# Performance work log

Hardware: AMD Instinct MI355X
Metric: run time of the kernel (lower is better)

Reference implementation:

```python
import jax, jax.numpy as jnp
import numpy as np
import math

B, T, D, NH, HD = 2, 1024, 768, 12, 64
V, L, E, CAP_F, H = 50257, 2, 8, 1.25, 2048
AUX_W, Z_W, THETA, EPS = 0.01, 0.001, 10000.0, 1e-5
N = B * T
CAP = int(math.ceil(N / E * CAP_F))  # 320


def setup_inputs():
    key = jax.random.key(0)
    ks = jax.random.split(key, 8)
    s = 0.02
    return dict(
        idx=jax.random.randint(ks[0], (B, T), 0, V),
        wte=jax.random.normal(ks[1], (V, D), jnp.float32) * s,
        wqkv=jax.random.normal(ks[2], (L, D, 3 * D), jnp.float32) * s,
        q_norm_w=jnp.ones((L, D), jnp.float32),
        k_norm_w=jnp.ones((L, D), jnp.float32),
        o_proj=jax.random.normal(ks[3], (L, D, D), jnp.float32) * s,
        ffn_norm_w=jnp.ones((L, D), jnp.float32),
        gate_w=jax.random.normal(ks[4], (L, D, E), jnp.float32) * s,
        w13=jax.random.normal(ks[5], (L, E, D, 2 * H), jnp.float32) * s,
        w2=jax.random.normal(ks[6], (L, E, H, D), jnp.float32) * s,
        ln_f_w=jnp.ones((D,), jnp.float32),
    )


def rmsnorm(x, w):
    return x * jax.lax.rsqrt(jnp.mean(x * x, axis=-1, keepdims=True) + EPS) * w


def rope(x, cos, sin):
    # x: (B, nh, T, HD) viewed as complex pairs on last dim
    xr = x.reshape(*x.shape[:-1], HD // 2, 2)
    x0, x1 = xr[..., 0], xr[..., 1]
    out = jnp.stack([x0 * cos - x1 * sin, x0 * sin + x1 * cos], axis=-1)
    return out.reshape(x.shape)


def moe(x, gate_w, w13, w2):
    # x: (B, T, D) -> Switch MoE (k=1) with capacity CAP and token drops
    x_flat = x.reshape(N, D).astype(jnp.float32)
    logits = x_flat @ gate_w  # (N, E) fp32
    probs = jax.nn.softmax(logits, axis=-1)
    top = jnp.argmax(logits, axis=-1)  # (N,)
    prob_mass = probs.mean(axis=0)
    fraction = jax.nn.one_hot(top, E, dtype=jnp.float32).mean(axis=0)
    balance_loss = jnp.sum(prob_mass * fraction) * AUX_W * E
    z = jax.nn.logsumexp(logits, axis=-1)
    z_loss = jnp.mean(z * z) * Z_W
    aux = balance_loss + z_loss

    sort_idx = jnp.argsort(top)  # stable
    sorted_assign = top[sort_idx]
    counts = jnp.bincount(sorted_assign, length=E)
    offsets = jnp.concatenate([jnp.zeros((1,), counts.dtype), jnp.cumsum(counts)])[:E]
    rank = jnp.arange(N) - offsets[sorted_assign]  # position within expert segment
    keep = rank < CAP
    x_perm = x_flat[sort_idx]
    slot = jnp.where(keep, rank, CAP)  # dropped -> overflow slot
    buf = jnp.zeros((E, CAP + 1, D), jnp.float32).at[sorted_assign, slot].set(x_perm)
    xb = buf[:, :CAP]  # (E, CAP, D)
    gu = jnp.einsum('ecd,edh->ech', xb, w13)  # (E, CAP, 2H)
    g, u = jnp.split(gu, 2, axis=-1)
    y = jnp.einsum('ech,ehd->ecd', jax.nn.silu(g) * u, w2)  # (E, CAP, D)
    out_perm = y[sorted_assign, jnp.minimum(rank, CAP - 1)] * keep[:, None]
    out_flat = jnp.zeros((N, D), jnp.float32).at[sort_idx].set(out_perm)
    return out_flat.reshape(B, T, D), aux, top.reshape(B, T), keep[jnp.argsort(sort_idx)].reshape(B, T)


def forward(idx, wte, wqkv, q_norm_w, k_norm_w, o_proj, ffn_norm_w, gate_w, w13, w2, ln_f_w):
    x = wte[idx]  # (B, T, D)
    freqs = 1.0 / (THETA ** (jnp.arange(0, HD, 2, dtype=jnp.float32) / HD))
    ang = jnp.outer(jnp.arange(T, dtype=jnp.float32), freqs)  # (T, HD//2)
    cos, sin = jnp.cos(ang)[None, None], jnp.sin(ang)[None, None]
    mask = jnp.where(jnp.tril(jnp.ones((T, T), bool)), 0.0, -jnp.inf)
    aux_total = jnp.float32(0.0)
    for l in range(L):
        qkv = x @ wqkv[l]
        q, k, v = jnp.split(qkv, 3, axis=-1)
        q = rmsnorm(q, q_norm_w[l])
        k = rmsnorm(k, k_norm_w[l])
        q = q.reshape(B, T, NH, HD).transpose(0, 2, 1, 3)
        k = k.reshape(B, T, NH, HD).transpose(0, 2, 1, 3)
        v = v.reshape(B, T, NH, HD).transpose(0, 2, 1, 3)
        q, k = rope(q, cos, sin), rope(k, cos, sin)
        scores = jnp.einsum('bhqd,bhkd->bhqk', q, k) / math.sqrt(HD) + mask
        attn = jax.nn.softmax(scores, axis=-1)
        y = jnp.einsum('bhqk,bhkd->bhqd', attn, v).transpose(0, 2, 1, 3).reshape(B, T, D)
        h = x + y @ o_proj[l]
        ffn_in = rmsnorm(h, ffn_norm_w[l])
        moe_out, aux, _, _ = moe(ffn_in, gate_w[l], w13[l], w2[l])
        aux_total = aux_total + aux
        x = h + moe_out
    x = rmsnorm(x, ln_f_w)
    logits = x @ wte.T  # tied lm_head
    return logits, aux_total


def reference(idx, wte, wqkv, q_norm_w, k_norm_w, o_proj, ffn_norm_w, gate_w, w13, w2, ln_f_w):
    return forward(idx, wte, wqkv, q_norm_w, k_norm_w, o_proj, ffn_norm_w, gate_w, w13, w2, ln_f_w)
```

## Files before the change

kernel.cpp:

```cpp
#include <hip/hip_runtime.h>

typedef __attribute__((ext_vector_type(8))) _Float16 half8;
typedef __attribute__((ext_vector_type(4))) float f32x4;

constexpr int Bc = 2, Tc = 1024, Dc = 768, NHc = 12, HDc = 64;
constexpr int Vc = 50257, Lc = 2, Ec = 8, Hc = 2048;
constexpr int Ntok = Bc * Tc;
constexpr int CAPc = 320, CAPPc = 384;
constexpr long long LOGITS_N = (long long)Bc * Tc * Vc;

typedef const __attribute__((address_space(1))) unsigned int* gas_t;
typedef __attribute__((address_space(3))) unsigned int* las_t;
__device__ __forceinline__ void gload16(const void* g, void* l) {
  __builtin_amdgcn_global_load_lds((gas_t)g, (las_t)l, 16, 0, 0);
}

__device__ __forceinline__ void splitf16(float a, unsigned short& h, unsigned short& l) {
  _Float16 hh = (_Float16)a;
  _Float16 ll = (_Float16)(a - (float)hh);
  h = __builtin_bit_cast(unsigned short, hh);
  l = __builtin_bit_cast(unsigned short, ll);
}
__device__ __forceinline__ unsigned short f16o(float a) {
  _Float16 hh = (_Float16)a;
  return __builtin_bit_cast(unsigned short, hh);
}


__global__ void zero_small(float* psum, float* z2) {
  int t = threadIdx.x;
  if (t < Lc * Ec) psum[t] = 0.f;
  if (t < Lc) z2[t] = 0.f;
}

__global__ void embed_k(const int* __restrict__ idx, const float* __restrict__ wte,
                        float* __restrict__ x, unsigned short* __restrict__ x16) {
  int n = blockIdx.x;
  long long v = idx[n];
  const float4* src = (const float4*)(wte + v * 768);
  float4* dst = (float4*)(x + (long long)n * 768);
  int t = threadIdx.x;
  if (t < 192) {
    float4 val = src[t];
    dst[t] = val;
    ushort4 h, l;
    splitf16(val.x, h.x, l.x); splitf16(val.y, h.y, l.y);
    splitf16(val.z, h.z, l.z); splitf16(val.w, h.w, l.w);
    unsigned short* d = x16 + (long long)n * 1536 + t * 4;
    *(ushort4*)d = h;
    *(ushort4*)(d + 768) = l;
  }
}

__global__ void f2h4(const float* __restrict__ in, unsigned short* __restrict__ out,
                     long long n4) {
  long long i = (long long)blockIdx.x * 256 + threadIdx.x;
  if (i >= n4) return;
  float4 v = ((const float4*)in)[i];
  ushort4 o;
  o.x = f16o(v.x); o.y = f16o(v.y); o.z = f16o(v.z); o.w = f16o(v.w);
  ((ushort4*)out)[i] = o;
}

template <int SP>
__global__ void __launch_bounds__(256) split2_wT(const float* __restrict__ src,
    unsigned short* __restrict__ dst, int K, int N, long long sS, long long sD) {
  __shared__ float t[32][33];
  int z = blockIdx.z;
  src += (long long)z * sS;
  dst += (long long)z * sD;
  int n0 = blockIdx.x * 32, k0 = blockIdx.y * 32;
  int tid = threadIdx.x;
  int r = tid >> 3, c4 = (tid & 7) * 4;
  float4 v = *(const float4*)(src + (long long)(k0 + r) * N + n0 + c4);
  t[r][c4 + 0] = v.x; t[r][c4 + 1] = v.y; t[r][c4 + 2] = v.z; t[r][c4 + 3] = v.w;
  __syncthreads();
  int n = tid >> 3, kq = (tid & 7) * 4;
  ushort4 h, l;
  splitf16(t[kq + 0][n], h.x, l.x);
  splitf16(t[kq + 1][n], h.y, l.y);
  splitf16(t[kq + 2][n], h.z, l.z);
  splitf16(t[kq + 3][n], h.w, l.w);
  const int lda = SP ? 2 * K : K;
  unsigned short* d = dst + (long long)(n0 + n) * lda + k0 + kq;
  *(ushort4*)d = h;
  if (SP) *(ushort4*)(d + K) = l;
}

__global__ void __launch_bounds__(256) rmsnorm_k(const float* in, int istride,
                                                 float* outp, int ostride,
                                                 const float* w) {
  long long n = blockIdx.x;
  const float* xr = in + n * istride;
  float* yr = outp + n * ostride;
  int tid = threadIdx.x;
  float s = 0.f;
  for (int i = tid; i < 768; i += 256) { float v = xr[i]; s += v * v; }
  #pragma unroll
  for (int o = 32; o; o >>= 1) s += __shfl_down(s, o);
  __shared__ float red[4];
  __shared__ float bs;
  if ((tid & 63) == 0) red[tid >> 6] = s;
  __syncthreads();
  if (tid == 0) bs = rsqrtf((red[0] + red[1] + red[2] + red[3]) / 768.0f + 1e-5f);
  __syncthreads();
  float sc = bs;
  for (int i = tid; i < 768; i += 256) yr[i] = xr[i] * sc * w[i];
}

__global__ void __launch_bounds__(256) rmsnorm_h(const float* in,
                                                 unsigned short* outp, const float* w) {
  long long n = blockIdx.x;
  const float* xr = in + n * 768;
  unsigned short* yr = outp + n * 768;
  int tid = threadIdx.x;
  float s = 0.f;
  for (int i = tid; i < 768; i += 256) { float v = xr[i]; s += v * v; }
  #pragma unroll
  for (int o = 32; o; o >>= 1) s += __shfl_down(s, o);
  __shared__ float red[4];
  __shared__ float bs;
  if ((tid & 63) == 0) red[tid >> 6] = s;
  __syncthreads();
  if (tid == 0) bs = rsqrtf((red[0] + red[1] + red[2] + red[3]) / 768.0f + 1e-5f);
  __syncthreads();
  float sc = bs;
  for (int i = tid; i < 768; i += 256) yr[i] = f16o(xr[i] * sc * w[i]);
}

__global__ void __launch_bounds__(256) qk_rope(const float* __restrict__ qkv,
    const float* __restrict__ qnw, const float* __restrict__ knw,
    unsigned short* __restrict__ qr, unsigned short* __restrict__ kr,
    unsigned short* __restrict__ vr) {
  int n = blockIdx.x;
  int t = n & 1023, b = n >> 10;
  const float* row = qkv + (long long)n * 2304;
  int tid = threadIdx.x;
  float sq = 0.f, sk = 0.f;
  for (int i = tid; i < 768; i += 256) {
    float q = row[i]; sq += q * q;
    float k = row[768 + i]; sk += k * k;
  }
  #pragma unroll
  for (int o = 32; o; o >>= 1) { sq += __shfl_down(sq, o); sk += __shfl_down(sk, o); }
  __shared__ float redq[4], redk[4];
  __shared__ float bq, bk;
  if ((tid & 63) == 0) { redq[tid >> 6] = sq; redk[tid >> 6] = sk; }
  __syncthreads();
  if (tid == 0) {
    bq = rsqrtf((redq[0] + redq[1] + redq[2] + redq[3]) / 768.0f + 1e-5f);
    bk = rsqrtf((redk[0] + redk[1] + redk[2] + redk[3]) / 768.0f + 1e-5f);
  }
  __syncthreads();
  float nq = bq, nk = bk;
  for (int i = tid; i < 384; i += 256) {
    int hh = i >> 5, j = i & 31;
    int c = hh * 64 + 2 * j;
    float ang = (float)t * powf(10000.0f, -((float)j * (1.0f / 32.0f)));
    float cs = cosf(ang), sn = sinf(ang);
    int z = b * 12 + hh;
    long long qb = ((long long)z * 1024 + t) * 128 + 2 * j;
    unsigned short h0, l0, h1, l1;
    float q0 = row[c] * nq * qnw[c], q1 = row[c + 1] * nq * qnw[c + 1];
    splitf16(q0 * cs - q1 * sn, h0, l0);
    splitf16(q0 * sn + q1 * cs, h1, l1);
    *(unsigned int*)&qr[qb] = (unsigned)h0 | ((unsigned)h1 << 16);
    *(unsigned int*)&qr[qb + 64] = (unsigned)l0 | ((unsigned)l1 << 16);
    float k0 = row[768 + c] * nk * knw[c], k1 = row[768 + c + 1] * nk * knw[c + 1];
    splitf16(k0 * cs - k1 * sn, h0, l0);
    splitf16(k0 * sn + k1 * cs, h1, l1);
    *(unsigned int*)&kr[qb] = (unsigned)h0 | ((unsigned)h1 << 16);
    *(unsigned int*)&kr[qb + 64] = (unsigned)l0 | ((unsigned)l1 << 16);
    splitf16(row[1536 + c], h0, l0);
    splitf16(row[1536 + c + 1], h1, l1);
    long long vb = ((long long)z * 64 + 2 * j) * 2048 + t;
    vr[vb] = h0; vr[vb + 1024] = l0;
    vr[vb + 2048] = h1; vr[vb + 3072] = l1;
  }
}

__global__ void __launch_bounds__(256) flash_attn(
    const unsigned short* __restrict__ qr, const unsigned short* __restrict__ kr,
    const unsigned short* __restrict__ vr, unsigned short* __restrict__ yout) {
  __shared__ __align__(16) unsigned short Ph[4][16][72];
  __shared__ __align__(16) unsigned short Pl[4][16][72];
  int bid = blockIdx.x;
  int z = bid >> 4;
  int qt = 15 - (bid & 15);
  int b = z / 12, h = z % 12;
  int q0 = qt * 64;
  int wave = threadIdx.x >> 6, lane = threadIdx.x & 63;
  int lr = lane & 15, lg = lane >> 4;
  int qw = q0 + wave * 16;
  half8 af[2][2];
  const unsigned short* qbase = qr + ((long long)z * 1024 + qw + lr) * 128;
  #pragma unroll
  for (int ks = 0; ks < 2; ++ks)
    #pragma unroll
    for (int p = 0; p < 2; ++p)
      af[ks][p] = *(const half8*)(qbase + p * 64 + ks * 32 + lg * 8);
  f32x4 accy[4];
  #pragma unroll
  for (int df = 0; df < 4; ++df) accy[df] = (f32x4){0.f, 0.f, 0.f, 0.f};
  float mrun[4] = {-3.4e38f, -3.4e38f, -3.4e38f, -3.4e38f};
  float srun[4] = {0.f, 0.f, 0.f, 0.f};
  for (int kt = 0; kt <= qt; ++kt) {
    int kv0 = kt * 64;
    f32x4 s[4];
    #pragma unroll
    for (int nf = 0; nf < 4; ++nf) s[nf] = (f32x4){0.f, 0.f, 0.f, 0.f};
    const unsigned short* kbase = kr + ((long long)z * 1024 + kv0 + lr) * 128;
    #pragma unroll
    for (int nf = 0; nf < 4; ++nf) {
      const unsigned short* kb = kbase + nf * 16 * 128;
      #pragma unroll
      for (int ks = 0; ks < 2; ++ks) {
        half8 bh = *(const half8*)(kb + ks * 32 + lg * 8);
        half8 bl = *(const half8*)(kb + 64 + ks * 32 + lg * 8);
        s[nf] = __builtin_amdgcn_mfma_f32_16x16x32_f16(af[ks][0], bh, s[nf], 0, 0, 0);
        s[nf] = __builtin_amdgcn_mfma_f32_16x16x32_f16(af[ks][1], bh, s[nf], 0, 0, 0);
        s[nf] = __builtin_amdgcn_mfma_f32_16x16x32_f16(af[ks][0], bl, s[nf], 0, 0, 0);
      }
    }
    bool diag = (kt == qt);
    #pragma unroll
    for (int nf = 0; nf < 4; ++nf)
      #pragma unroll
      for (int j = 0; j < 4; ++j) {
        float v = s[nf][j] * 0.125f;
        if (diag && (nf * 16 + lr > wave * 16 + lg * 4 + j)) v = -1e30f;
        s[nf][j] = v;
      }
    #pragma unroll
    for (int j = 0; j < 4; ++j) {
      float tm = fmaxf(fmaxf(s[0][j], s[1][j]), fmaxf(s[2][j], s[3][j]));
      #pragma unroll
      for (int o = 1; o < 16; o <<= 1) tm = fmaxf(tm, __shfl_xor(tm, o));
      float mnew = fmaxf(mrun[j], tm);
      float sc = expf(mrun[j] - mnew);
      float ts = 0.f;
      #pragma unroll
      for (int nf = 0; nf < 4; ++nf) {
        float p = expf(s[nf][j] - mnew);
        ts += p;
        unsigned short ph, pl;
        splitf16(p, ph, pl);
        Ph[wave][lg * 4 + j][nf * 16 + lr] = ph;
        Pl[wave][lg * 4 + j][nf * 16 + lr] = pl;
      }
      #pragma unroll
      for (int o = 1; o < 16; o <<= 1) ts += __shfl_xor(ts, o);
      srun[j] = srun[j] * sc + ts;
      mrun[j] = mnew;
      #pragma unroll
      for (int df = 0; df < 4; ++df) accy[df][j] *= sc;
    }
    #pragma unroll
    for (int ks2 = 0; ks2 < 2; ++ks2) {
      half8 aph = *(const half8*)&Ph[wave][lr][ks2 * 32 + lg * 8];
      half8 apl = *(const half8*)&Pl[wave][lr][ks2 * 32 + lg * 8];
      #pragma unroll
      for (int df = 0; df < 4; ++df) {
        const unsigned short* vb =
            vr + ((long long)z * 64 + df * 16 + lr) * 2048 + kv0 + ks2 * 32 + lg * 8;
        half8 bvh = *(const half8*)vb;
        half8 bvl = *(const half8*)(vb + 1024);
        accy[df] = __builtin_amdgcn_mfma_f32_16x16x32_f16(aph, bvh, accy[df], 0, 0, 0);
        accy[df] = __builtin_amdgcn_mfma_f32_16x16x32_f16(apl, bvh, accy[df], 0, 0, 0);
        accy[df] = __builtin_amdgcn_mfma_f32_16x16x32_f16(aph, bvl, accy[df], 0, 0, 0);
      }
    }
  }
  float inv[4];
  #pragma unroll
  for (int j = 0; j < 4; ++j) inv[j] = 1.0f / srun[j];
  #pragma unroll
  for (int df = 0; df < 4; ++df)
    #pragma unroll
    for (int j = 0; j < 4; ++j) {
      long long tok = (long long)b * 1024 + qw + lg * 4 + j;
      int col = h * 64 + df * 16 + lr;
      unsigned short hh, ll;
      splitf16(accy[df][j] * inv[j], hh, ll);
      yout[tok * 1536 + col] = hh;
      yout[tok * 1536 + 768 + col] = ll;
    }
}

__global__ void __launch_bounds__(256) gate_k(const float* __restrict__ xin,
    const float* __restrict__ gw, int* __restrict__ top,
    float* __restrict__ psum, float* __restrict__ z2) {
  __shared__ float gws[768 * 8];
  __shared__ float pacc[8];
  __shared__ float zacc;
  int tid = threadIdx.x;
  for (int i = tid; i < 768 * 8 / 4; i += 256) ((float4*)gws)[i] = ((const float4*)gw)[i];
  if (tid < 8) pacc[tid] = 0.f;
  if (tid == 0) zacc = 0.f;
  __syncthreads();
  int n = blockIdx.x * 256 + tid;
  const float4* xr4 = (const float4*)(xin + (long long)n * 768);
  float l[8] = {0, 0, 0, 0, 0, 0, 0, 0};
  for (int d4 = 0; d4 < 192; ++d4) {
    float4 xv = xr4[d4];
    const float* g = &gws[d4 * 32];
    #pragma unroll
    for (int e = 0; e < 8; ++e)
      l[e] += xv.x * g[e] + xv.y * g[8 + e] + xv.z * g[16 + e] + xv.w * g[24 + e];
  }
  float mx = l[0]; int bi = 0;
  #pragma unroll
  for (int e = 1; e < 8; ++e) if (l[e] > mx) { mx = l[e]; bi = e; }
  float p[8]; float se = 0.f;
  #pragma unroll
  for (int e = 0; e < 8; ++e) { p[e] = expf(l[e] - mx); se += p[e]; }
  float z = mx + logf(se);
  top[n] = bi;
  #pragma unroll
  for (int e = 0; e < 8; ++e) atomicAdd(&pacc[e], p[e] / se);
  atomicAdd(&zacc, z * z);
  __syncthreads();
  if (tid < 8) atomicAdd(&psum[tid], pacc[tid]);
  if (tid == 0) atomicAdd(z2, zacc);
}

__global__ void route_scan(const int* __restrict__ top, int* __restrict__ rank,
                           int* __restrict__ cnt) {
  int lane = threadIdx.x;
  int c[8] = {0, 0, 0, 0, 0, 0, 0, 0};
  unsigned long long below = (1ull << lane) - 1ull;
  for (int s = 0; s < Ntok / 64; ++s) {
    int n = s * 64 + lane;
    int e = top[n];
    int r = 0;
    #pragma unroll
    for (int q = 0; q < 8; ++q) {
      unsigned long long m = __ballot(e == q);
      if (e == q) r = c[q] + __popcll(m & below);
      c[q] += __popcll(m);
    }
    rank[n] = r;
  }
  #pragma unroll
  for (int q = 0; q < 8; ++q) if (lane == q) cnt[q] = c[q];
}

template <int SP>
__global__ void scatter_xb(const float* __restrict__ xin, const int* __restrict__ top,
                           const int* __restrict__ rank, unsigned short* __restrict__ xb) {
  int n = blockIdx.x;
  int r = rank[n];
  if (r >= CAPc) return;
  int e = top[n];
  int t = threadIdx.x;
  if (t >= 192) return;
  float4 v = ((const float4*)(xin + (long long)n * 768))[t];
  ushort4 h, l;
  splitf16(v.x, h.x, l.x); splitf16(v.y, h.y, l.y);
  splitf16(v.z, h.z, l.z); splitf16(v.w, h.w, l.w);
  const int lda = SP ? 1536 : 768;
  unsigned short* dst = xb + ((long long)e * CAPPc + r) * lda + t * 4;
  *(ushort4*)dst = h;
  if (SP) *(ushort4*)(dst + 768) = l;
}

template <int SP>
__global__ void __launch_bounds__(256) silu_k(const float* __restrict__ gu,
                                              unsigned short* __restrict__ act) {
  long long i = (long long)blockIdx.x * 256 + threadIdx.x;
  long long row = i >> 11;
  int h = (int)(i & 2047);
  float g = gu[row * 4096 + h];
  float u = gu[row * 4096 + 2048 + h];
  float a = g / (1.f + expf(-g)) * u;
  if (SP) {
    unsigned short hh, ll;
    splitf16(a, hh, ll);
    act[row * 4096 + h] = hh;
    act[row * 4096 + 2048 + h] = ll;
  } else {
    act[row * 2048 + h] = f16o(a);
  }
}

__global__ void gather_add(const float* __restrict__ h, const float* __restrict__ yexp,
                           const int* __restrict__ top, const int* __restrict__ rank,
                           float* __restrict__ xo, unsigned short* __restrict__ x16) {
  int n = blockIdx.x;
  int r = rank[n], e = top[n];
  bool kept = r < CAPc;
  int rc = kept ? r : (CAPc - 1);
  const float4* hs = (const float4*)(h + (long long)n * 768);
  const float4* ys = (const float4*)(yexp + ((long long)e * CAPPc + rc) * 768);
  float4* dst = (float4*)(xo + (long long)n * 768);
  int t = threadIdx.x;
  if (t < 192) {
    float4 v = hs[t];
    if (kept) { float4 y = ys[t]; v.x += y.x; v.y += y.y; v.z += y.z; v.w += y.w; }
    dst[t] = v;
    ushort4 hh, ll;
    splitf16(v.x, hh.x, ll.x); splitf16(v.y, hh.y, ll.y);
    splitf16(v.z, hh.z, ll.z); splitf16(v.w, hh.w, ll.w);
    unsigned short* d = x16 + (long long)n * 1536 + t * 4;
    *(ushort4*)d = hh;
    *(ushort4*)(d + 768) = ll;
  }
}

__global__ void aux_fin(const float* __restrict__ psum, const int* __restrict__ cnt,
                        const float* __restrict__ z2, float* __restrict__ outp) {
  if (threadIdx.x == 0) {
    float aux = 0.f;
    for (int l = 0; l < Lc; ++l) {
      float bl = 0.f;
      for (int e = 0; e < 8; ++e)
        bl += (psum[l * 8 + e] * (1.0f / 2048.0f)) * ((float)cnt[l * 8 + e] * (1.0f / 2048.0f));
      aux += bl * (0.01f * 8.0f) + (z2[l] * (1.0f / 2048.0f)) * 0.001f;
    }
    outp[0] = aux;
  }
}

template <int BN, int SPLIT, int ADD, int NTAIL>
__global__ void __launch_bounds__(256) gemm_h(
    const unsigned short* __restrict__ A, const unsigned short* __restrict__ Bt,
    float* __restrict__ C, const float* __restrict__ Add,
    int M, int N, int K, int ldc, int gx, int gy,
    long long sA, long long sB, int zdiv, long long sC1, long long sC2) {
  constexpr int FN = (BN == 128) ? 4 : 2;
  constexpr int APL = 128 * 32;
  constexpr int BPL = BN * 32;
  constexpr int BUF = 2 * APL + 2 * BPL;
  __shared__ __align__(16) unsigned short lds[2][BUF];
  int tot = gridDim.x;
  int lin = blockIdx.x;
  if ((tot & 7) == 0) lin = (lin & 7) * (tot >> 3) + (lin >> 3);
  int pz = lin / (gx * gy);
  int r2 = lin - pz * (gx * gy);
  const int m0 = (r2 % gx) * 128, n0 = (r2 / gx) * BN;
  A += (long long)pz * sA;
  Bt += (long long)pz * sB;
  const long long co = (long long)(pz / zdiv) * sC1 + (long long)(pz % zdiv) * sC2;
  const int lda = SPLIT ? 2 * K : K;
  const int NS = SPLIT ? K / 32 : K / 64;
  const int tid = threadIdx.x;
  const int lane = tid & 63, wave = tid >> 6;
  const int wm = (BN == 128) ? (wave >> 1) : (wave & 1);
  const int wn = (BN == 128) ? (wave & 1) : (wave >> 1);
  const int srow = tid >> 2, scol = (tid & 3) * 8;
  const unsigned short* Ar = A + (long long)(m0 + srow) * lda + scol;
  int br0 = n0 + srow;
  if (NTAIL) br0 = min(br0, N - 1);
  const unsigned short* Br = Bt + (long long)br0 * lda + scol;
  int br1 = n0 + srow + 64;
  if (NTAIL) br1 = min(br1, N - 1);
  const unsigned short* Br2 = Bt + (long long)br1 * lda + scol;

  auto STAGE = [&](int buf, int s) {
    const int kh = SPLIT ? s * 32 : s * 64;
    const int kl = SPLIT ? K + s * 32 : s * 64 + 32;
    unsigned short* L = lds[buf];
    gload16(Ar + kh, &L[wave * 512]);
    gload16(Ar + (long long)64 * lda + kh, &L[2048 + wave * 512]);
    gload16(Ar + kl, &L[APL + wave * 512]);
    gload16(Ar + (long long)64 * lda + kl, &L[APL + 2048 + wave * 512]);
    gload16(Br + kh, &L[2 * APL + wave * 512]);
    gload16(Br + kl, &L[2 * APL + BPL + wave * 512]);
    if (BN == 128) {
      gload16(Br2 + kh, &L[2 * APL + 2048 + wave * 512]);
      gload16(Br2 + kl, &L[2 * APL + BPL + 2048 + wave * 512]);
    }
  };

  f32x4 acc[4][FN];
  #pragma unroll
  for (int m = 0; m < 4; ++m)
    #pragma unroll
    for (int n = 0; n < FN; ++n) acc[m][n] = (f32x4){0.f, 0.f, 0.f, 0.f};

  STAGE(0, 0);
  int cur = 0;
  for (int s = 0; s < NS; ++s) {
    if (s + 1 < NS) {
      STAGE(cur ^ 1, s + 1);
      if constexpr (BN == 128)
        asm volatile("s_waitcnt vmcnt(8)" ::: "memory");
      else
        asm volatile("s_waitcnt vmcnt(6)" ::: "memory");
    } else {
      asm volatile("s_waitcnt vmcnt(0)" ::: "memory");
    }
    __builtin_amdgcn_sched_barrier(0);
    __builtin_amdgcn_s_barrier();
    const unsigned short* L = lds[cur];
    half8 bfh[FN], bfl[FN];
    #pragma unroll
    for (int n = 0; n < FN; ++n) {
      int bo = (wn * (FN * 16) + n * 16 + (lane & 15)) * 32 + (lane >> 4) * 8;
      bfh[n] = *(const half8*)&L[2 * APL + bo];
      bfl[n] = *(const half8*)&L[2 * APL + BPL + bo];
    }
    __builtin_amdgcn_s_setprio(1);
    #pragma unroll
    for (int m = 0; m < 4; ++m) {
      int ao = (wm * 64 + m * 16 + (lane & 15)) * 32 + (lane >> 4) * 8;
      half8 afh = *(const half8*)&L[ao];
      half8 afl = *(const half8*)&L[APL + ao];
      #pragma unroll
      for (int n = 0; n < FN; ++n) {
        acc[m][n] = __builtin_amdgcn_mfma_f32_16x16x32_f16(afh, bfh[n], acc[m][n], 0, 0, 0);
        if (SPLIT) {
          acc[m][n] = __builtin_amdgcn_mfma_f32_16x16x32_f16(afl, bfh[n], acc[m][n], 0, 0, 0);
          acc[m][n] = __builtin_amdgcn_mfma_f32_16x16x32_f16(afh, bfl[n], acc[m][n], 0, 0, 0);
        } else {
          acc[m][n] = __builtin_amdgcn_mfma_f32_16x16x32_f16(afl, bfl[n], acc[m][n], 0, 0, 0);
        }
      }
    }
    __builtin_amdgcn_s_setprio(0);
    __builtin_amdgcn_sched_barrier(0);
    __builtin_amdgcn_s_barrier();
    cur ^= 1;
  }
  #pragma unroll
  for (int m = 0; m < 4; ++m)
    #pragma unroll
    for (int n = 0; n < FN; ++n) {
      int col = n0 + wn * (FN * 16) + n * 16 + (lane & 15);
      if (!NTAIL || col < N) {
        #pragma unroll
        for (int j = 0; j < 4; ++j) {
          long long row = m0 + wm * 64 + m * 16 + (lane >> 4) * 4 + j;
          long long o = co + row * ldc + col;
          float v = acc[m][n][j];
          if (ADD) v += Add[o];
          C[o] = v;
        }
      }
    }
}

__global__ void __launch_bounds__(512) gemm_logits(
    const unsigned short* __restrict__ A, const unsigned short* __restrict__ Bt,
    float* __restrict__ C, int M, int N, int K, int ldc, int gx) {
  constexpr int BUFS = 24576;
  constexpr int BOFF = 16384;
  __shared__ __align__(16) unsigned short lds[3 * BUFS];
  int tot = gridDim.x;
  int lin = blockIdx.x;
  if ((tot & 7) == 0) lin = (lin & 7) * (tot >> 3) + (lin >> 3);
  const int m0 = (lin % gx) * 256, n0 = (lin / gx) * 128;
  const int tid = threadIdx.x;
  const int lane = tid & 63;
  const int wm = (tid >> 6) >> 1, wn = (tid >> 6) & 1;
  const int NS = K / 64;

  auto STAGE = [&](int buf, int t) {
    const int k0 = t * 64;
    unsigned short* L = lds + buf * BUFS;
    #pragma unroll
    for (int i = 0; i < 4; ++i) {
      int idx = tid + i * 512;
      int row = idx >> 3, blk = idx & 7;
      gload16(A + (long long)(m0 + row) * K + k0 + ((blk ^ (row & 7)) << 3),
              L + idx * 8);
    }
    #pragma unroll
    for (int i = 0; i < 2; ++i) {
      int idx = tid + i * 512;
      int row = idx >> 3, blk = idx & 7;
      int br = min(n0 + row, N - 1);
      gload16(Bt + (long long)br * K + k0 + ((blk ^ (row & 7)) << 3),
              L + BOFF + idx * 8);
    }
  };

  f32x4 acc[4][4];
  #pragma unroll
  for (int mf = 0; mf < 4; ++mf)
    #pragma unroll
    for (int nf = 0; nf < 4; ++nf) acc[mf][nf] = (f32x4){0.f, 0.f, 0.f, 0.f};

  STAGE(0, 0); STAGE(1, 1); STAGE(2, 2);
  for (int s = 0; s < NS; ++s) {
    if (s + 3 <= NS)      asm volatile("s_waitcnt vmcnt(12)" ::: "memory");
    else if (s + 2 <= NS) asm volatile("s_waitcnt vmcnt(6)" ::: "memory");
    else                  asm volatile("s_waitcnt vmcnt(0)" ::: "memory");
    __builtin_amdgcn_sched_barrier(0);
    __builtin_amdgcn_s_barrier();
    const unsigned short* L = lds + (s % 3) * BUFS;
    half8 a[4][2], b[4][2];
    #pragma unroll
    for (int mf = 0; mf < 4; ++mf)
      #pragma unroll
      for (int ks = 0; ks < 2; ++ks) {
        int row = wm * 64 + mf * 16 + (lane & 15);
        int blk = (ks * 4 + (lane >> 4)) ^ (row & 7);
        a[mf][ks] = *(const half8*)(L + row * 64 + blk * 8);
      }
    #pragma unroll
    for (int nf = 0; nf < 4; ++nf)
      #pragma unroll
      for (int ks = 0; ks < 2; ++ks) {
        int row = wn * 64 + nf * 16 + (lane & 15);
        int blk = (ks * 4 + (lane >> 4)) ^ (row & 7);
        b[nf][ks] = *(const half8*)(L + BOFF + row * 64 + blk * 8);
      }
    asm volatile("s_waitcnt lgkmcnt(0)" ::: "memory");
    __builtin_amdgcn_sched_barrier(0);
    __builtin_amdgcn_s_barrier();
    if (s + 3 < NS) STAGE((s + 3) % 3, s + 3);
    __builtin_amdgcn_s_setprio(1);
    #pragma unroll
    for (int ks = 0; ks < 2; ++ks)
      #pragma unroll
      for (int mf = 0; mf < 4; ++mf)
        #pragma unroll
        for (int nf = 0; nf < 4; ++nf)
          acc[mf][nf] = __builtin_amdgcn_mfma_f32_16x16x32_f16(a[mf][ks], b[nf][ks],
                                                               acc[mf][nf], 0, 0, 0);
    __builtin_amdgcn_s_setprio(0);
  }
  #pragma unroll
  for (int mf = 0; mf < 4; ++mf)
    #pragma unroll
    for (int nf = 0; nf < 4; ++nf) {
      int col = n0 + wn * 64 + nf * 16 + (lane & 15);
      if (col < N) {
        #pragma unroll
        for (int j = 0; j < 4; ++j) {
          long long row = m0 + wm * 64 + mf * 16 + (lane >> 4) * 4 + j;
          C[row * (long long)ldc + col] = acc[mf][nf][j];
        }
      }
    }
}


extern "C" void kernel_launch(void* const* d_in, const int* in_sizes, int n_in,
                              void* d_out, int out_size, void* d_ws, size_t ws_size,
                              hipStream_t stream) {
  (void)in_sizes; (void)n_in; (void)out_size; (void)ws_size;
  const int*   idx   = (const int*)d_in[0];
  const float* wte   = (const float*)d_in[1];
  const float* wqkv  = (const float*)d_in[2];
  const float* qnw   = (const float*)d_in[3];
  const float* knw   = (const float*)d_in[4];
  const float* oproj = (const float*)d_in[5];
  const float* ffnw  = (const float*)d_in[6];
  const float* gatew = (const float*)d_in[7];
  const float* w13   = (const float*)d_in[8];
  const float* w2p   = (const float*)d_in[9];
  const float* lnf   = (const float*)d_in[10];
  float* out = (float*)d_out;

  char* base = (char*)d_ws;
  size_t off = 0;
  auto alloc = [&](size_t bytes) -> char* {
    off = (off + 255) & ~(size_t)255;
    char* p = base + off; off += bytes; return p;
  };
  float* x     = (float*)alloc((size_t)Ntok * 768 * 4);
  float* qkv   = (float*)alloc((size_t)Ntok * 2304 * 4);
  float* hbuf  = (float*)alloc((size_t)Ntok * 768 * 4);
  float* ffn   = (float*)alloc((size_t)Ntok * 768 * 4);
  unsigned short* x16   = (unsigned short*)alloc((size_t)Ntok * 1536 * 2);
  unsigned short* yfl16 = (unsigned short*)alloc((size_t)Ntok * 1536 * 2);
  unsigned short* qr16  = (unsigned short*)alloc((size_t)24 * 1024 * 128 * 2);
  unsigned short* kr16  = (unsigned short*)alloc((size_t)24 * 1024 * 128 * 2);
  unsigned short* vr16  = (unsigned short*)alloc((size_t)24 * 64 * 2048 * 2);
  unsigned short* xb16  = (unsigned short*)alloc((size_t)Ec * CAPPc * 1536 * 2);
  unsigned short* wo16  = (unsigned short*)alloc((size_t)768 * 1536 * 2);
  unsigned short* xf16  = (unsigned short*)alloc((size_t)Ntok * 768 * 2);
  char* spb = alloc((size_t)24 * 1024 * 1024 * 4);
  float* gu   = (float*)spb;
  float* yexp = (float*)spb;
  unsigned short* act16 = (unsigned short*)(spb + 50331648);
  unsigned short* wq16  = (unsigned short*)(spb + 75497472);
  unsigned short* w13_16 = (unsigned short*)alloc((size_t)Ec * 4096 * 1536 * 2);
  unsigned short* wt16   = w13_16;
  unsigned short* w2_16  = (unsigned short*)alloc((size_t)Ec * 768 * 4096 * 2);
  int* top    = (int*)alloc(Ntok * 4);
  int* rankb  = (int*)alloc(Ntok * 4);
  int* cnt    = (int*)alloc(Lc * Ec * 4);
  float* psum = (float*)alloc(Lc * Ec * 4);
  float* z2   = (float*)alloc(Lc * 4);

  zero_small<<<1, 64, 0, stream>>>(psum, z2);
  embed_k<<<Ntok, 192, 0, stream>>>(idx, wte, x, x16);

  for (int l = 0; l < Lc; ++l) {
    split2_wT<1><<<dim3(72, 24, 1), 256, 0, stream>>>(wqkv + (size_t)l * 768 * 2304, wq16,
                                                      768, 2304, 0, 0);
    split2_wT<1><<<dim3(24, 24, 1), 256, 0, stream>>>(oproj + (size_t)l * 768 * 768, wo16,
                                                      768, 768, 0, 0);
    if (l == 0) {
      split2_wT<1><<<dim3(128, 24, 8), 256, 0, stream>>>(w13, w13_16,
          768, 4096, (long long)768 * 4096, (long long)4096 * 1536);
      split2_wT<1><<<dim3(24, 64, 8), 256, 0, stream>>>(w2p, w2_16,
          2048, 768, (long long)2048 * 768, (long long)768 * 4096);
    } else {
      split2_wT<0><<<dim3(128, 24, 8), 256, 0, stream>>>(w13 + (size_t)Ec * 768 * 4096, w13_16,
          768, 4096, (long long)768 * 4096, (long long)4096 * 768);
      split2_wT<0><<<dim3(24, 64, 8), 256, 0, stream>>>(w2p + (size_t)Ec * 2048 * 768, w2_16,
          2048, 768, (long long)2048 * 768, (long long)768 * 2048);
    }
    gemm_h<128, 1, 0, 0><<<288, 256, 0, stream>>>(
        x16, wq16, qkv, nullptr, 2048, 2304, 768, 2304, 16, 18, 0, 0, 1, 0, 0);
    qk_rope<<<Ntok, 256, 0, stream>>>(qkv, qnw + l * 768, knw + l * 768, qr16, kr16, vr16);
    flash_attn<<<384, 256, 0, stream>>>(qr16, kr16, vr16, yfl16);
    gemm_h<64, 1, 1, 0><<<192, 256, 0, stream>>>(
        yfl16, wo16, hbuf, x, 2048, 768, 768, 768, 16, 12, 0, 0, 1, 0, 0);
    rmsnorm_k<<<Ntok, 256, 0, stream>>>(hbuf, 768, ffn, 768, ffnw + l * 768);
    gate_k<<<Ntok / 256, 256, 0, stream>>>(ffn, gatew + (size_t)l * 768 * 8, top,
                                           psum + l * 8, z2 + l);
    route_scan<<<1, 64, 0, stream>>>(top, rankb, cnt + l * 8);
    if (l == 0) {
      scatter_xb<1><<<Ntok, 192, 0, stream>>>(ffn, top, rankb, xb16);
      gemm_h<128, 1, 0, 0><<<768, 256, 0, stream>>>(
          xb16, w13_16, gu, nullptr, 384, 4096, 768, 4096, 3, 32,
          (long long)384 * 1536, (long long)4096 * 1536, 1, (long long)384 * 4096, 0);
      silu_k<1><<<(Ec * CAPPc * Hc) / 256, 256, 0, stream>>>(gu, act16);
      gemm_h<64, 1, 0, 0><<<288, 256, 0, stream>>>(
          act16, w2_16, yexp, nullptr, 384, 768, 2048, 768, 3, 12,
          (long long)384 * 4096, (long long)768 * 4096, 1, (long long)384 * 768, 0);
    } else {
      scatter_xb<0><<<Ntok, 192, 0, stream>>>(ffn, top, rankb, xb16);
      gemm_h<128, 0, 0, 0><<<768, 256, 0, stream>>>(
          xb16, w13_16, gu, nullptr, 384, 4096, 768, 4096, 3, 32,
          (long long)384 * 768, (long long)4096 * 768, 1, (long long)384 * 4096, 0);
      silu_k<0><<<(Ec * CAPPc * Hc) / 256, 256, 0, stream>>>(gu, act16);
      gemm_h<64, 0, 0, 0><<<288, 256, 0, stream>>>(
          act16, w2_16, yexp, nullptr, 384, 768, 2048, 768, 3, 12,
          (long long)384 * 2048, (long long)768 * 2048, 1, (long long)384 * 768, 0);
    }
    gather_add<<<Ntok, 192, 0, stream>>>(hbuf, yexp, top, rankb, x, x16);
  }

  rmsnorm_h<<<Ntok, 256, 0, stream>>>(x, xf16, lnf);
  f2h4<<<(int)(((long long)Vc * 768 / 4 + 255) / 256), 256, 0, stream>>>(
      wte, wt16, (long long)Vc * 768 / 4);
  gemm_logits<<<8 * 393, 512, 0, stream>>>(xf16, wt16, out, 2048, Vc, 768, Vc, 8);
  aux_fin<<<1, 64, 0, stream>>>(psum, cnt, z2, out + LOGITS_N);
}
```

Measured before the change: 1.304 ms.

## Fuse SiLU into expert up-projection GEMM epilogue and restructure LDS pipelining

Interleaves the gate and up columns of w13 during weight conversion, so each GEMM tile holds matching gate/up pairs. The GEMM epilogue can then apply SiLU and write the fp16 (split or single) activation directly, removing the fp32 gu buffer round trip and the separate silu kernel. It also reorders the double-buffer staging in gemm_h to wait fully and then issue the next stage after the barrier, dropping one barrier per iteration. gemm_logits moves from a three-deep to a two-deep prefetch, issued after the barrier, which removes a second barrier per step. The shallower prefetch may expose more memory latency in both GEMMs.

New measurement: 1.253 ms. 1.04x faster.

```diff
diff --git a/kernel.cpp b/kernel.cpp
--- a/kernel.cpp
+++ b/kernel.cpp
@@ -62,7 +62,7 @@
   ((ushort4*)out)[i] = o;
 }
 
-template <int SP>
+template <int SP, int ILV>
 __global__ void __launch_bounds__(256) split2_wT(const float* __restrict__ src,
     unsigned short* __restrict__ dst, int K, int N, long long sS, long long sD) {
   __shared__ float t[32][33];
@@ -82,7 +82,12 @@
   splitf16(t[kq + 2][n], h.z, l.z);
   splitf16(t[kq + 3][n], h.w, l.w);
   const int lda = SP ? 2 * K : K;
-  unsigned short* d = dst + (long long)(n0 + n) * lda + k0 + kq;
+  int nd = n0 + n;
+  if (ILV) {
+    int hh = nd & 2047, iu = nd >> 11;
+    nd = ((hh >> 4) << 5) + (iu << 4) + (hh & 15);
+  }
+  unsigned short* d = dst + (long long)nd * lda + k0 + kq;
   *(ushort4*)d = h;
   if (SP) *(ushort4*)(d + K) = l;
 }
@@ -364,25 +369,6 @@
   if (SP) *(ushort4*)(dst + 768) = l;
 }
 
-template <int SP>
-__global__ void __launch_bounds__(256) silu_k(const float* __restrict__ gu,
-                                              unsigned short* __restrict__ act) {
-  long long i = (long long)blockIdx.x * 256 + threadIdx.x;
-  long long row = i >> 11;
-  int h = (int)(i & 2047);
-  float g = gu[row * 4096 + h];
-  float u = gu[row * 4096 + 2048 + h];
-  float a = g / (1.f + expf(-g)) * u;
-  if (SP) {
-    unsigned short hh, ll;
-    splitf16(a, hh, ll);
-    act[row * 4096 + h] = hh;
-    act[row * 4096 + 2048 + h] = ll;
-  } else {
-    act[row * 2048 + h] = f16o(a);
-  }
-}
-
 __global__ void gather_add(const float* __restrict__ h, const float* __restrict__ yexp,
                            const int* __restrict__ top, const int* __restrict__ rank,
                            float* __restrict__ xo, unsigned short* __restrict__ x16) {
@@ -421,7 +407,7 @@
   }
 }
 
-template <int BN, int SPLIT, int ADD, int NTAIL>
+template <int BN, int SPLIT, int ADD, int NTAIL, int SILU>
 __global__ void __launch_bounds__(256) gemm_h(
     const unsigned short* __restrict__ A, const unsigned short* __restrict__ Bt,
     float* __restrict__ C, const float* __restrict__ Add,
@@ -481,17 +467,10 @@
   STAGE(0, 0);
   int cur = 0;
   for (int s = 0; s < NS; ++s) {
-    if (s + 1 < NS) {
-      STAGE(cur ^ 1, s + 1);
-      if constexpr (BN == 128)
-        asm volatile("s_waitcnt vmcnt(8)" ::: "memory");
-      else
-        asm volatile("s_waitcnt vmcnt(6)" ::: "memory");
-    } else {
-      asm volatile("s_waitcnt vmcnt(0)" ::: "memory");
-    }
+    asm volatile("s_waitcnt vmcnt(0)" ::: "memory");
     __builtin_amdgcn_sched_barrier(0);
     __builtin_amdgcn_s_barrier();
+    if (s + 1 < NS) STAGE(cur ^ 1, s + 1);
     const unsigned short* L = lds[cur];
     half8 bfh[FN], bfl[FN];
     #pragma unroll
@@ -518,26 +497,50 @@
       }
     }
     __builtin_amdgcn_s_setprio(0);
-    __builtin_amdgcn_sched_barrier(0);
-    __builtin_amdgcn_s_barrier();
     cur ^= 1;
   }
-  #pragma unroll
-  for (int m = 0; m < 4; ++m)
-    #pragma unroll
-    for (int n = 0; n < FN; ++n) {
-      int col = n0 + wn * (FN * 16) + n * 16 + (lane & 15);
-      if (!NTAIL || col < N) {
+  if constexpr (SILU) {
+    unsigned short* act = (unsigned short*)C;
+    #pragma unroll
+    for (int m = 0; m < 4; ++m)
+      #pragma unroll
+      for (int p = 0; p < FN / 2; ++p) {
+        f32x4 g = acc[m][2 * p], u = acc[m][2 * p + 1];
+        int colh = ((n0 + wn * (FN * 16)) >> 1) + p * 16 + (lane & 15);
         #pragma unroll
         for (int j = 0; j < 4; ++j) {
           long long row = m0 + wm * 64 + m * 16 + (lane >> 4) * 4 + j;
-          long long o = co + row * ldc + col;
-          float v = acc[m][n][j];
-          if (ADD) v += Add[o];
-          C[o] = v;
+          float gv = g[j];
+          float a = gv / (1.f + expf(-gv)) * u[j];
+          long long o = co + row * ldc + colh;
+          if (SILU == 1) {
+            unsigned short hh, ll;
+            splitf16(a, hh, ll);
+            act[o] = hh;
+            act[o + 2048] = ll;
+          } else {
+            act[o] = f16o(a);
+          }
         }
       }
-    }
+  } else {
+    #pragma unroll
+    for (int m = 0; m < 4; ++m)
+      #pragma unroll
+      for (int n = 0; n < FN; ++n) {
+        int col = n0 + wn * (FN * 16) + n * 16 + (lane & 15);
+        if (!NTAIL || col < N) {
+          #pragma unroll
+          for (int j = 0; j < 4; ++j) {
+            long long row = m0 + wm * 64 + m * 16 + (lane >> 4) * 4 + j;
+            long long o = co + row * ldc + col;
+            float v = acc[m][n][j];
+            if (ADD) v += Add[o];
+            C[o] = v;
+          }
+        }
+      }
+  }
 }
 
 __global__ void __launch_bounds__(512) gemm_logits(
@@ -581,13 +584,13 @@
     #pragma unroll
     for (int nf = 0; nf < 4; ++nf) acc[mf][nf] = (f32x4){0.f, 0.f, 0.f, 0.f};
 
-  STAGE(0, 0); STAGE(1, 1); STAGE(2, 2);
+  STAGE(0, 0); STAGE(1, 1);
   for (int s = 0; s < NS; ++s) {
-    if (s + 3 <= NS)      asm volatile("s_waitcnt vmcnt(12)" ::: "memory");
-    else if (s + 2 <= NS) asm volatile("s_waitcnt vmcnt(6)" ::: "memory");
-    else                  asm volatile("s_waitcnt vmcnt(0)" ::: "memory");
+    if (s + 1 < NS) asm volatile("s_waitcnt vmcnt(6)" ::: "memory");
+    else            asm volatile("s_waitcnt vmcnt(0)" ::: "memory");
     __builtin_amdgcn_sched_barrier(0);
     __builtin_amdgcn_s_barrier();
+    if (s + 2 < NS) STAGE((s + 2) % 3, s + 2);
     const unsigned short* L = lds + (s % 3) * BUFS;
     half8 a[4][2], b[4][2];
     #pragma unroll
@@ -606,10 +609,6 @@
         int blk = (ks * 4 + (lane >> 4)) ^ (row & 7);
         b[nf][ks] = *(const half8*)(L + BOFF + row * 64 + blk * 8);
       }
-    asm volatile("s_waitcnt lgkmcnt(0)" ::: "memory");
-    __builtin_amdgcn_sched_barrier(0);
-    __builtin_amdgcn_s_barrier();
-    if (s + 3 < NS) STAGE((s + 3) % 3, s + 3);
     __builtin_amdgcn_s_setprio(1);
     #pragma unroll
     for (int ks = 0; ks < 2; ++ks)
@@ -673,7 +672,6 @@
   unsigned short* wo16  = (unsigned short*)alloc((size_t)768 * 1536 * 2);
   unsigned short* xf16  = (unsigned short*)alloc((size_t)Ntok * 768 * 2);
   char* spb = alloc((size_t)24 * 1024 * 1024 * 4);
-  float* gu   = (float*)spb;
   float* yexp = (float*)spb;
   unsigned short* act16 = (unsigned short*)(spb + 50331648);
   unsigned short* wq16  = (unsigned short*)(spb + 75497472);
@@ -690,26 +688,26 @@
   embed_k<<<Ntok, 192, 0, stream>>>(idx, wte, x, x16);
 
   for (int l = 0; l < Lc; ++l) {
-    split2_wT<1><<<dim3(72, 24, 1), 256, 0, stream>>>(wqkv + (size_t)l * 768 * 2304, wq16,
-                                                      768, 2304, 0, 0);
-    split2_wT<1><<<dim3(24, 24, 1), 256, 0, stream>>>(oproj + (size_t)l * 768 * 768, wo16,
-                                                      768, 768, 0, 0);
+    split2_wT<1, 0><<<dim3(72, 24, 1), 256, 0, stream>>>(wqkv + (size_t)l * 768 * 2304,
+                                                         wq16, 768, 2304, 0, 0);
+    split2_wT<1, 0><<<dim3(24, 24, 1), 256, 0, stream>>>(oproj + (size_t)l * 768 * 768,
+                                                         wo16, 768, 768, 0, 0);
     if (l == 0) {
-      split2_wT<1><<<dim3(128, 24, 8), 256, 0, stream>>>(w13, w13_16,
+      split2_wT<1, 1><<<dim3(128, 24, 8), 256, 0, stream>>>(w13, w13_16,
           768, 4096, (long long)768 * 4096, (long long)4096 * 1536);
-      split2_wT<1><<<dim3(24, 64, 8), 256, 0, stream>>>(w2p, w2_16,
+      split2_wT<1, 0><<<dim3(24, 64, 8), 256, 0, stream>>>(w2p, w2_16,
           2048, 768, (long long)2048 * 768, (long long)768 * 4096);
     } else {
-      split2_wT<0><<<dim3(128, 24, 8), 256, 0, stream>>>(w13 + (size_t)Ec * 768 * 4096, w13_16,
-          768, 4096, (long long)768 * 4096, (long long)4096 * 768);
-      split2_wT<0><<<dim3(24, 64, 8), 256, 0, stream>>>(w2p + (size_t)Ec * 2048 * 768, w2_16,
-          2048, 768, (long long)2048 * 768, (long long)768 * 2048);
-    }
-    gemm_h<128, 1, 0, 0><<<288, 256, 0, stream>>>(
+      split2_wT<0, 1><<<dim3(128, 24, 8), 256, 0, stream>>>(w13 + (size_t)Ec * 768 * 4096,
+          w13_16, 768, 4096, (long long)768 * 4096, (long long)4096 * 768);
+      split2_wT<0, 0><<<dim3(24, 64, 8), 256, 0, stream>>>(w2p + (size_t)Ec * 2048 * 768,
+          w2_16, 2048, 768, (long long)2048 * 768, (long long)768 * 2048);
+    }
+    gemm_h<128, 1, 0, 0, 0><<<288, 256, 0, stream>>>(
         x16, wq16, qkv, nullptr, 2048, 2304, 768, 2304, 16, 18, 0, 0, 1, 0, 0);
     qk_rope<<<Ntok, 256, 0, stream>>>(qkv, qnw + l * 768, knw + l * 768, qr16, kr16, vr16);
     flash_attn<<<384, 256, 0, stream>>>(qr16, kr16, vr16, yfl16);
-    gemm_h<64, 1, 1, 0><<<192, 256, 0, stream>>>(
+    gemm_h<64, 1, 1, 0, 0><<<192, 256, 0, stream>>>(
         yfl16, wo16, hbuf, x, 2048, 768, 768, 768, 16, 12, 0, 0, 1, 0, 0);
     rmsnorm_k<<<Ntok, 256, 0, stream>>>(hbuf, 768, ffn, 768, ffnw + l * 768);
     gate_k<<<Ntok / 256, 256, 0, stream>>>(ffn, gatew + (size_t)l * 768 * 8, top,
@@ -717,20 +715,18 @@
     route_scan<<<1, 64, 0, stream>>>(top, rankb, cnt + l * 8);
     if (l == 0) {
       scatter_xb<1><<<Ntok, 192, 0, stream>>>(ffn, top, rankb, xb16);
-      gemm_h<128, 1, 0, 0><<<768, 256, 0, stream>>>(
-          xb16, w13_16, gu, nullptr, 384, 4096, 768, 4096, 3, 32,
+      gemm_h<128, 1, 0, 0, 1><<<768, 256, 0, stream>>>(
+          xb16, w13_16, (float*)act16, nullptr, 384, 4096, 768, 4096, 3, 32,
           (long long)384 * 1536, (long long)4096 * 1536, 1, (long long)384 * 4096, 0);
-      silu_k<1><<<(Ec * CAPPc * Hc) / 256, 256, 0, stream>>>(gu, act16);
-      gemm_h<64, 1, 0, 0><<<288, 256, 0, stream>>>(
+      gemm_h<64, 1, 0, 0, 0><<<288, 256, 0, stream>>>(
           act16, w2_16, yexp, nullptr, 384, 768, 2048, 768, 3, 12,
           (long long)384 * 4096, (long long)768 * 4096, 1, (long long)384 * 768, 0);
     } else {
       scatter_xb<0><<<Ntok, 192, 0, stream>>>(ffn, top, rankb, xb16);
-      gemm_h<128, 0, 0, 0><<<768, 256, 0, stream>>>(
-          xb16, w13_16, gu, nullptr, 384, 4096, 768, 4096, 3, 32,
-          (long long)384 * 768, (long long)4096 * 768, 1, (long long)384 * 4096, 0);
-      silu_k<0><<<(Ec * CAPPc * Hc) / 256, 256, 0, stream>>>(gu, act16);
-      gemm_h<64, 0, 0, 0><<<288, 256, 0, stream>>>(
+      gemm_h<128, 0, 0, 0, 2><<<768, 256, 0, stream>>>(
+          xb16, w13_16, (float*)act16, nullptr, 384, 4096, 768, 2048, 3, 32,
+          (long long)384 * 768, (long long)4096 * 768, 1, (long long)384 * 2048, 0);
+      gemm_h<64, 0, 0, 0, 0><<<288, 256, 0, stream>>>(
           act16, w2_16, yexp, nullptr, 384, 768, 2048, 768, 3, 12,
           (long long)384 * 2048, (long long)768 * 2048, 1, (long long)384 * 768, 0);
     }
```
